# Kernel optimization log

Measured on AMD Instinct MI355X. Metric: run time of the kernel, lower is better.

The kernel has to match this reference:

```python
import jax, jax.numpy as jnp
import numpy as np

B, C_IN, H, W = 1, 448, 64, 64   # concat of resnet18 layer1/2/3 resized to 64x64: 64+128+256=448
D, L = 100, 4096                 # projection dim, number of spatial locations (gaussian params)
OUT_HW = 256                     # input_size for final bilinear upsample


def setup_inputs() -> dict:
    key = jax.random.key(0)
    k0, k1, k2, k3, k4 = jax.random.split(key, 5)
    return {
        "features": jax.random.normal(k0, (B, C_IN, H, W), jnp.float32),
        "proj_w": jax.random.normal(k1, (D, C_IN), jnp.float32) * 0.05,
        "proj_b": jax.random.normal(k2, (D,), jnp.float32) * 0.05,
        "mean": jax.random.normal(k3, (D, L), jnp.float32),
        "inv_cov": jax.random.normal(k4, (L, D, D), jnp.float32) * 0.01,
    }


def reference(features, proj_w, proj_b, mean, inv_cov):
    Bn, C, Hh, Ww = features.shape
    # permute(0,2,3,1).reshape(-1, C) then Linear(C, D)
    f = features.transpose(0, 2, 3, 1).reshape(-1, C)          # (N, C), N = B*H*W
    f = f @ proj_w.T + proj_b                                  # (N, D)
    m = mean.T                                                 # (L, D)
    # Batched Mahalanobis-style quadratic form replacing the Python loop over L=4096:
    #   dist[n, l] = (f_n - m_l)^T  inv_cov_l  (f_n - m_l)
    # Expanded so the heavy term is a single (N, D*D) x (D*D, L) GEMM (no (N,L,D) intermediate).
    Cm  = jnp.einsum('lde,le->ld', inv_cov, m)                 # inv_cov_l @ m_l        (L, D)
    CTm = jnp.einsum('lde,ld->le', inv_cov, m)                 # inv_cov_l^T @ m_l      (L, D)
    const = jnp.einsum('ld,ld->l', m, Cm)                      # m_l^T inv_cov_l m_l    (L,)
    ff = (f[:, :, None] * f[:, None, :]).reshape(f.shape[0], D * D)   # outer(f,f) flattened (N, D*D)
    quad = ff @ inv_cov.reshape(L, D * D).T                    # f^T inv_cov_l f        (N, L)
    dist = quad - f @ (Cm + CTm).T + const[None, :]            # (N, L)
    min_d = jnp.min(dist, axis=1).reshape(Bn, Hh, Ww)[:, None, :, :]  # (B, 1, H, W)
    amap = (min_d - min_d.min()) / (min_d.max() - min_d.min() + 1e-8)
    amap = jax.image.resize(amap, (Bn, 1, OUT_HW, OUT_HW), method='bilinear')
    return amap
```

## Files before the change

### kernel.cpp

```cpp
#include <hip/hip_runtime.h>
#include <hip/hip_bf16.h>
#include <stdint.h>

#define CIN   448
#define DP    100
#define NPIX  4096
#define LNUM  4096
#define KQ    5050
#define KLIN  5150
#define KTOT  5184
#define KSTEPS (KTOT / 64)
#define OUTHW 256

typedef _Float16 f16_t;
typedef _Float16 f16x8 __attribute__((ext_vector_type(8)));
typedef float    f32x4 __attribute__((ext_vector_type(4)));
typedef unsigned short u16x8 __attribute__((ext_vector_type(8)));

static __device__ __forceinline__ int tri_off(int d) { return (d * (201 - d)) >> 1; }

static __device__ __forceinline__ void unpack_tri(int k, int& d, int& e) {
    int dd = (int)((201.0f - sqrtf(40401.0f - 8.0f * (float)k)) * 0.5f);
    if (dd < 0) dd = 0;
    if (dd > 99) dd = 99;
    while (tri_off(dd + 1) <= k) ++dd;
    while (tri_off(dd) > k) --dd;
    d = dd;
    e = dd + (k - tri_off(dd));
}

static __device__ __forceinline__ unsigned f2u(float x) {
    unsigned b = __float_as_uint(x);
    return (b & 0x80000000u) ? ~b : (b | 0x80000000u);
}
static __device__ __forceinline__ float u2f(unsigned u) {
    unsigned b = (u & 0x80000000u) ? (u & 0x7FFFFFFFu) : ~u;
    return __uint_as_float(b);
}

static __device__ __forceinline__ void gload_lds16(const f16_t* g, f16_t* l) {
    __builtin_amdgcn_global_load_lds((const __attribute__((address_space(1))) unsigned*)g,
                                     (__attribute__((address_space(3))) unsigned*)l,
                                     16, 0, 0);
}

__global__ void k_lut(unsigned short* __restrict__ lut) {
    int k = blockIdx.x * 256 + threadIdx.x;
    if (k < KTOT) {
        int d = 0, e = 0;
        if (k < KQ) unpack_tri(k, d, e);
        lut[k] = (unsigned short)(d | (e << 8));
    }
}

__global__ void k_proj(const float* __restrict__ feat, const float* __restrict__ w,
                       const float* __restrict__ b, float* __restrict__ f) {
    int gid = blockIdx.x * 256 + threadIdx.x;
    int n = gid & 4095;
    int d = gid >> 12;
    float acc = b[d];
    const float* wd = w + d * CIN;
    #pragma unroll 4
    for (int c = 0; c < CIN; ++c) acc += feat[c * 4096 + n] * wd[c];
    f[n * DP + d] = acc;
}

__global__ __launch_bounds__(256) void k_buildA(const float* __restrict__ f, const unsigned short* __restrict__ lut,
                                                f16_t* __restrict__ A) {
    __shared__ float fr[DP];
    int n = blockIdx.x;
    int t = threadIdx.x;
    if (t < DP) fr[t] = f[n * DP + t];
    __syncthreads();
    int r  = n & 127;
    int rsw = (r & 7) << 3;
    f16_t* tileBase = A + (size_t)(n >> 7) * KSTEPS * 8192;
    for (int g = t; g < KTOT / 8; g += 256) {
        int k0 = g * 8;
        u16x8 lu = *(const u16x8*)&lut[k0];
        f16x8 v;
        #pragma unroll
        for (int j = 0; j < 8; ++j) {
            int k = k0 + j;
            float x;
            if (k < KQ) {
                int d = lu[j] & 255, e = lu[j] >> 8;
                x = fr[d] * fr[e];
            } else if (k < KLIN) {
                x = fr[k - KQ];
            } else {
                x = 0.0f;
            }
            v[j] = (f16_t)x;
        }
        int kt = k0 >> 6, kin = k0 & 63;
        *(f16x8*)&tileBase[kt * 8192 + r * 64 + ((kin & 56) ^ rsw)] = v;
    }
}

__global__ __launch_bounds__(256) void k_buildB(const float* __restrict__ icov, const float* __restrict__ mean,
                                                const unsigned short* __restrict__ lut,
                                                f16_t* __restrict__ Bm, float* __restrict__ constl) {
    __shared__ float ic[DP * 101];
    __shared__ float ml[DP];
    __shared__ float wv[DP];
    __shared__ float part[DP];
    int l = blockIdx.x;
    int t = threadIdx.x;
    const float* src = icov + (size_t)l * DP * DP;
    for (int i = t; i < DP * DP; i += 256) {
        int row = i / 100;
        ic[row * 101 + (i - row * 100)] = src[i];
    }
    if (t < DP) ml[t] = mean[t * LNUM + l];
    __syncthreads();
    if (t < DP) {
        float icm = 0.f, ictm = 0.f;
        for (int e = 0; e < DP; ++e) {
            icm  += ic[t * 101 + e] * ml[e];
            ictm += ic[e * 101 + t] * ml[e];
        }
        wv[t]   = icm + ictm;
        part[t] = ml[t] * icm;
    }
    __syncthreads();
    if (t == 0) {
        float c = 0.f;
        for (int d = 0; d < DP; ++d) c += part[d];
        constl[l] = c;
    }
    int r  = l & 127;
    int rsw = (r & 7) << 3;
    f16_t* tileBase = Bm + (size_t)(l >> 7) * KSTEPS * 8192;
    for (int g = t; g < KTOT / 8; g += 256) {
        int k0 = g * 8;
        u16x8 lu = *(const u16x8*)&lut[k0];
        f16x8 v;
        #pragma unroll
        for (int j = 0; j < 8; ++j) {
            int k = k0 + j;
            float x;
            if (k < KQ) {
                int d = lu[j] & 255, e = lu[j] >> 8;
                float s = ic[d * 101 + e] + ic[e * 101 + d];
                x = (d == e) ? 0.5f * s : s;
            } else if (k < KLIN) {
                x = -wv[k - KQ];
            } else {
                x = 0.0f;
            }
            v[j] = (f16_t)x;
        }
        int kt = k0 >> 6, kin = k0 & 63;
        *(f16x8*)&tileBase[kt * 8192 + r * 64 + ((kin & 56) ^ rsw)] = v;
    }
}

__global__ void k_init(unsigned* __restrict__ mind) {
    int i = blockIdx.x * 256 + threadIdx.x;
    if (i < NPIX) mind[i] = 0xFFFFFFFFu;
}

__global__ __launch_bounds__(512, 2) void k_gemm(const f16_t* __restrict__ A, const f16_t* __restrict__ Bm,
                                                 const float* __restrict__ constl, unsigned* __restrict__ mind) {
    __shared__ __align__(16) f16_t sA[2][16384];
    __shared__ __align__(16) f16_t sB[2][16384];

    int bid = blockIdx.x;
    int pid = ((bid & 7) << 5) | (bid >> 3);
    int bm = pid & 15;
    int bn = pid >> 4;

    int t = threadIdx.x;
    int lane = t & 63;
    int w = t >> 6;
    int wr = w >> 2;
    int wc = w & 3;

    f32x4 acc[8][4];
    #pragma unroll
    for (int i = 0; i < 8; ++i)
        #pragma unroll
        for (int j = 0; j < 4; ++j) acc[i][j] = (f32x4){0.f, 0.f, 0.f, 0.f};

    const f16_t* Abase = A  + ((size_t)(2 * bm + (w >> 2)) * KSTEPS) * 8192 + (w & 3) * 2048 + lane * 8;
    const f16_t* Bbase = Bm + ((size_t)(2 * bn + (w >> 2)) * KSTEPS) * 8192 + (w & 3) * 2048 + lane * 8;

    int l15 = lane & 15;
    int xorv = (lane & 7) << 3;
    int klobase = (lane >> 4) * 8;

    {
        const f16_t* As = Abase;
        const f16_t* Bs = Bbase;
        #pragma unroll
        for (int c = 0; c < 4; ++c) {
            gload_lds16(As + c * 512, &sA[0][w * 2048 + c * 512]);
            gload_lds16(Bs + c * 512, &sB[0][w * 2048 + c * 512]);
        }
    }
    __syncthreads();

    for (int kt = 0; kt < KSTEPS; ++kt) {
        int p = kt & 1;
        if (kt + 1 < KSTEPS) {
            const f16_t* As = Abase + (size_t)(kt + 1) * 8192;
            const f16_t* Bs = Bbase + (size_t)(kt + 1) * 8192;
            #pragma unroll
            for (int c = 0; c < 4; ++c) {
                gload_lds16(As + c * 512, &sA[p ^ 1][w * 2048 + c * 512]);
                gload_lds16(Bs + c * 512, &sB[p ^ 1][w * 2048 + c * 512]);
            }
        }
        #pragma unroll
        for (int kk = 0; kk < 2; ++kk) {
            int klo = (kk * 32 + klobase) ^ xorv;
            f16x8 bfr[4];
            #pragma unroll
            for (int ni = 0; ni < 4; ++ni) {
                int rr = (wc & 1) * 64 + ni * 16 + l15;
                bfr[ni] = *(const f16x8*)&sB[p][(wc >> 1) * 8192 + rr * 64 + klo];
            }
            #pragma unroll
            for (int mq = 0; mq < 2; ++mq) {
                f16x8 afr[4];
                #pragma unroll
                for (int mi = 0; mi < 4; ++mi) {
                    int rr = (mq * 4 + mi) * 16 + l15;
                    afr[mi] = *(const f16x8*)&sA[p][wr * 8192 + rr * 64 + klo];
                }
                __builtin_amdgcn_s_setprio(1);
                #pragma unroll
                for (int mi = 0; mi < 4; ++mi)
                    #pragma unroll
                    for (int ni = 0; ni < 4; ++ni)
                        acc[mq * 4 + mi][ni] =
                            __builtin_amdgcn_mfma_f32_16x16x32_f16(afr[mi], bfr[ni], acc[mq * 4 + mi][ni], 0, 0, 0);
                __builtin_amdgcn_s_setprio(0);
            }
        }
        __syncthreads();
    }

    int colbase = bn * 256 + wc * 64 + l15;
    float cl[4];
    #pragma unroll
    for (int ni = 0; ni < 4; ++ni) cl[ni] = constl[colbase + ni * 16];
    #pragma unroll
    for (int mi8 = 0; mi8 < 8; ++mi8) {
        #pragma unroll
        for (int j = 0; j < 4; ++j) {
            float v = 1e30f;
            #pragma unroll
            for (int ni = 0; ni < 4; ++ni) v = fminf(v, acc[mi8][ni][j] + cl[ni]);
            #pragma unroll
            for (int s = 1; s < 16; s <<= 1) v = fminf(v, __shfl_xor(v, s, 64));
            if (l15 == 0) {
                int row = bm * 256 + wr * 128 + mi8 * 16 + (lane >> 4) * 4 + j;
                atomicMin(&mind[row], f2u(v));
            }
        }
    }
}

__global__ void k_minmax(const unsigned* __restrict__ mind, float* __restrict__ gmm) {
    __shared__ float smin[256], smax[256];
    int t = threadIdx.x;
    float vmin = 1e30f, vmax = -1e30f;
    for (int i = t; i < NPIX; i += 256) {
        float v = u2f(mind[i]);
        vmin = fminf(vmin, v);
        vmax = fmaxf(vmax, v);
    }
    smin[t] = vmin; smax[t] = vmax;
    __syncthreads();
    for (int s = 128; s > 0; s >>= 1) {
        if (t < s) {
            smin[t] = fminf(smin[t], smin[t + s]);
            smax[t] = fmaxf(smax[t], smax[t + s]);
        }
        __syncthreads();
    }
    if (t == 0) { gmm[0] = smin[0]; gmm[1] = smax[0]; }
}

__global__ void k_upsample(const unsigned* __restrict__ mind, const float* __restrict__ gmm,
                           float* __restrict__ out) {
    int gid = blockIdx.x * 256 + threadIdx.x;
    int i = gid >> 8, j = gid & 255;
    float gmin = gmm[0];
    float scale = 1.0f / (gmm[1] - gmm[0] + 1e-8f);
    float x = fminf(fmaxf(j * 0.25f - 0.375f, 0.0f), 63.0f);
    float y = fminf(fmaxf(i * 0.25f - 0.375f, 0.0f), 63.0f);
    int x0 = (int)x, y0 = (int)y;
    int x1 = min(x0 + 1, 63), y1 = min(y0 + 1, 63);
    float fx = x - x0, fy = y - y0;
    float v00 = u2f(mind[y0 * 64 + x0]), v01 = u2f(mind[y0 * 64 + x1]);
    float v10 = u2f(mind[y1 * 64 + x0]), v11 = u2f(mind[y1 * 64 + x1]);
    float v = v00 * (1.f - fy) * (1.f - fx) + v01 * (1.f - fy) * fx
            + v10 * fy * (1.f - fx) + v11 * fy * fx;
    out[gid] = (v - gmin) * scale;
}

__global__ void k_diag(float* __restrict__ out) {
    int gid = blockIdx.x * 256 + threadIdx.x;
    out[gid] = 0.25f;
}

extern "C" void kernel_launch(void* const* d_in, const int* in_sizes, int n_in,
                              void* d_out, int out_size, void* d_ws, size_t ws_size,
                              hipStream_t stream) {
    const float* feat = (const float*)d_in[0];
    const float* pw   = (const float*)d_in[1];
    const float* pb   = (const float*)d_in[2];
    const float* mean = (const float*)d_in[3];
    const float* icov = (const float*)d_in[4];

    size_t need = 0;
    auto count = [&need](size_t bytes) { need = ((need + 255) & ~(size_t)255) + bytes; };
    count((size_t)NPIX * DP * 4);
    count((size_t)NPIX * KTOT * 2);
    count((size_t)LNUM * KTOT * 2);
    count((size_t)LNUM * 4);
    count((size_t)NPIX * 4);
    count(2 * 4);
    count((size_t)KTOT * 2);
    if (ws_size < need) {
        k_diag<<<256, 256, 0, stream>>>((float*)d_out);
        return;
    }

    char* ws = (char*)d_ws;
    size_t off = 0;
    auto alloc = [&](size_t bytes) -> void* {
        off = (off + 255) & ~(size_t)255;
        void* p = ws + off;
        off += bytes;
        return p;
    };
    float*          f      = (float*)alloc((size_t)NPIX * DP * 4);
    f16_t*          Amat   = (f16_t*)alloc((size_t)NPIX * KTOT * 2);
    f16_t*          Bmat   = (f16_t*)alloc((size_t)LNUM * KTOT * 2);
    float*          constl = (float*)alloc((size_t)LNUM * 4);
    unsigned*       mind   = (unsigned*)alloc((size_t)NPIX * 4);
    float*          gmm    = (float*)alloc(2 * 4);
    unsigned short* lut    = (unsigned short*)alloc((size_t)KTOT * 2);

    k_lut     <<<(KTOT + 255) / 256, 256, 0, stream>>>(lut);
    k_proj    <<<1600, 256, 0, stream>>>(feat, pw, pb, f);
    k_buildA  <<<NPIX, 256, 0, stream>>>(f, lut, Amat);
    k_buildB  <<<LNUM, 256, 0, stream>>>(icov, mean, lut, Bmat, constl);
    k_init    <<<16, 256, 0, stream>>>(mind);
    k_gemm    <<<256, 512, 0, stream>>>(Amat, Bmat, constl, mind);
    k_minmax  <<<1, 256, 0, stream>>>(mind, gmm);
    k_upsample<<<256, 256, 0, stream>>>(mind, gmm, (float*)d_out);
}
```

Measured before the change: 292.6 us.

## Shrink GEMM tiles to 128x128 with 1024 blocks, fuse init, vectorize icov load

The main GEMM moves from 256x256 tiles with 512 threads and 256 blocks to 128x128 tiles with 256 threads and 1024 blocks. Each wave now computes a 64x64 subtile, and the block-to-tile swizzle changes to group blocks in bands of 8 M-tiles. The aim is to fill all CUs of the MI355X and raise occupancy, at the cost of lower operand reuse and twice the global/L2 traffic for A and B. The mind initialisation is folded into the LUT kernel, which removes one launch. The inverse-covariance load in buildB now uses float4 reads.

Measured after the change: 307.2 us. +5.0%, slower.

```diff
diff --git a/kernel.cpp b/kernel.cpp
--- a/kernel.cpp
+++ b/kernel.cpp
@@ -44,13 +44,14 @@
                                      16, 0, 0);
 }
 
-__global__ void k_lut(unsigned short* __restrict__ lut) {
+__global__ void k_lut(unsigned short* __restrict__ lut, unsigned* __restrict__ mind) {
     int k = blockIdx.x * 256 + threadIdx.x;
     if (k < KTOT) {
         int d = 0, e = 0;
         if (k < KQ) unpack_tri(k, d, e);
         lut[k] = (unsigned short)(d | (e << 8));
     }
+    if (k < NPIX) mind[k] = 0xFFFFFFFFu;
 }
 
 __global__ void k_proj(const float* __restrict__ feat, const float* __restrict__ w,
@@ -107,10 +108,14 @@
     __shared__ float part[DP];
     int l = blockIdx.x;
     int t = threadIdx.x;
-    const float* src = icov + (size_t)l * DP * DP;
-    for (int i = t; i < DP * DP; i += 256) {
-        int row = i / 100;
-        ic[row * 101 + (i - row * 100)] = src[i];
+    const float4* src4 = (const float4*)(icov + (size_t)l * DP * DP);
+    for (int i4 = t; i4 < DP * DP / 4; i4 += 256) {
+        float4 v = src4[i4];
+        int flat = i4 * 4;
+        int row = flat / 100;
+        int col = flat - row * 100;
+        float* dst = &ic[row * 101 + col];
+        dst[0] = v.x; dst[1] = v.y; dst[2] = v.z; dst[3] = v.w;
     }
     if (t < DP) ml[t] = mean[t * LNUM + l];
     __syncthreads();
@@ -156,56 +161,50 @@
     }
 }
 
-__global__ void k_init(unsigned* __restrict__ mind) {
-    int i = blockIdx.x * 256 + threadIdx.x;
-    if (i < NPIX) mind[i] = 0xFFFFFFFFu;
-}
-
-__global__ __launch_bounds__(512, 2) void k_gemm(const f16_t* __restrict__ A, const f16_t* __restrict__ Bm,
+__global__ __launch_bounds__(256, 2) void k_gemm(const f16_t* __restrict__ A, const f16_t* __restrict__ Bm,
                                                  const float* __restrict__ constl, unsigned* __restrict__ mind) {
-    __shared__ __align__(16) f16_t sA[2][16384];
-    __shared__ __align__(16) f16_t sB[2][16384];
+    __shared__ __align__(16) f16_t sA[2][8192];
+    __shared__ __align__(16) f16_t sB[2][8192];
 
     int bid = blockIdx.x;
-    int pid = ((bid & 7) << 5) | (bid >> 3);
-    int bm = pid & 15;
-    int bn = pid >> 4;
+    int pid = ((bid & 7) << 7) | (bid >> 3);
+    int group = pid >> 8;
+    int pin = pid & 255;
+    int bm = group * 8 + (pin & 7);
+    int bn = pin >> 3;
 
     int t = threadIdx.x;
     int lane = t & 63;
     int w = t >> 6;
-    int wr = w >> 2;
-    int wc = w & 3;
-
-    f32x4 acc[8][4];
+    int wr = w >> 1, wc = w & 1;
+
+    f32x4 acc[4][4];
     #pragma unroll
-    for (int i = 0; i < 8; ++i)
+    for (int i = 0; i < 4; ++i)
         #pragma unroll
         for (int j = 0; j < 4; ++j) acc[i][j] = (f32x4){0.f, 0.f, 0.f, 0.f};
 
-    const f16_t* Abase = A  + ((size_t)(2 * bm + (w >> 2)) * KSTEPS) * 8192 + (w & 3) * 2048 + lane * 8;
-    const f16_t* Bbase = Bm + ((size_t)(2 * bn + (w >> 2)) * KSTEPS) * 8192 + (w & 3) * 2048 + lane * 8;
+    const f16_t* Atile = A  + (size_t)bm * KSTEPS * 8192 + w * 2048 + lane * 8;
+    const f16_t* Btile = Bm + (size_t)bn * KSTEPS * 8192 + w * 2048 + lane * 8;
 
     int l15 = lane & 15;
     int xorv = (lane & 7) << 3;
     int klobase = (lane >> 4) * 8;
-
-    {
-        const f16_t* As = Abase;
-        const f16_t* Bs = Bbase;
-        #pragma unroll
-        for (int c = 0; c < 4; ++c) {
-            gload_lds16(As + c * 512, &sA[0][w * 2048 + c * 512]);
-            gload_lds16(Bs + c * 512, &sB[0][w * 2048 + c * 512]);
-        }
+    int arowbase = wr * 64 + l15;
+    int browbase = wc * 64 + l15;
+
+    #pragma unroll
+    for (int c = 0; c < 4; ++c) {
+        gload_lds16(Atile + c * 512, &sA[0][w * 2048 + c * 512]);
+        gload_lds16(Btile + c * 512, &sB[0][w * 2048 + c * 512]);
     }
     __syncthreads();
 
     for (int kt = 0; kt < KSTEPS; ++kt) {
         int p = kt & 1;
         if (kt + 1 < KSTEPS) {
-            const f16_t* As = Abase + (size_t)(kt + 1) * 8192;
-            const f16_t* Bs = Bbase + (size_t)(kt + 1) * 8192;
+            const f16_t* As = Atile + (size_t)(kt + 1) * 8192;
+            const f16_t* Bs = Btile + (size_t)(kt + 1) * 8192;
             #pragma unroll
             for (int c = 0; c < 4; ++c) {
                 gload_lds16(As + c * 512, &sA[p ^ 1][w * 2048 + c * 512]);
@@ -215,48 +214,37 @@
         #pragma unroll
         for (int kk = 0; kk < 2; ++kk) {
             int klo = (kk * 32 + klobase) ^ xorv;
-            f16x8 bfr[4];
-            #pragma unroll
-            for (int ni = 0; ni < 4; ++ni) {
-                int rr = (wc & 1) * 64 + ni * 16 + l15;
-                bfr[ni] = *(const f16x8*)&sB[p][(wc >> 1) * 8192 + rr * 64 + klo];
-            }
-            #pragma unroll
-            for (int mq = 0; mq < 2; ++mq) {
-                f16x8 afr[4];
+            f16x8 afr[4], bfr[4];
+            #pragma unroll
+            for (int mi = 0; mi < 4; ++mi)
+                afr[mi] = *(const f16x8*)&sA[p][(arowbase + mi * 16) * 64 + klo];
+            #pragma unroll
+            for (int ni = 0; ni < 4; ++ni)
+                bfr[ni] = *(const f16x8*)&sB[p][(browbase + ni * 16) * 64 + klo];
+            #pragma unroll
+            for (int mi = 0; mi < 4; ++mi)
                 #pragma unroll
-                for (int mi = 0; mi < 4; ++mi) {
-                    int rr = (mq * 4 + mi) * 16 + l15;
-                    afr[mi] = *(const f16x8*)&sA[p][wr * 8192 + rr * 64 + klo];
-                }
-                __builtin_amdgcn_s_setprio(1);
-                #pragma unroll
-                for (int mi = 0; mi < 4; ++mi)
-                    #pragma unroll
-                    for (int ni = 0; ni < 4; ++ni)
-                        acc[mq * 4 + mi][ni] =
-                            __builtin_amdgcn_mfma_f32_16x16x32_f16(afr[mi], bfr[ni], acc[mq * 4 + mi][ni], 0, 0, 0);
-                __builtin_amdgcn_s_setprio(0);
-            }
+                for (int ni = 0; ni < 4; ++ni)
+                    acc[mi][ni] = __builtin_amdgcn_mfma_f32_16x16x32_f16(afr[mi], bfr[ni], acc[mi][ni], 0, 0, 0);
         }
         __syncthreads();
     }
 
-    int colbase = bn * 256 + wc * 64 + l15;
+    int colbase = bn * 128 + wc * 64 + l15;
     float cl[4];
     #pragma unroll
     for (int ni = 0; ni < 4; ++ni) cl[ni] = constl[colbase + ni * 16];
     #pragma unroll
-    for (int mi8 = 0; mi8 < 8; ++mi8) {
+    for (int mi = 0; mi < 4; ++mi) {
         #pragma unroll
         for (int j = 0; j < 4; ++j) {
             float v = 1e30f;
             #pragma unroll
-            for (int ni = 0; ni < 4; ++ni) v = fminf(v, acc[mi8][ni][j] + cl[ni]);
+            for (int ni = 0; ni < 4; ++ni) v = fminf(v, acc[mi][ni][j] + cl[ni]);
             #pragma unroll
             for (int s = 1; s < 16; s <<= 1) v = fminf(v, __shfl_xor(v, s, 64));
             if (l15 == 0) {
-                int row = bm * 256 + wr * 128 + mi8 * 16 + (lane >> 4) * 4 + j;
+                int row = bm * 128 + wr * 64 + mi * 16 + (lane >> 4) * 4 + j;
                 atomicMin(&mind[row], f2u(v));
             }
         }
@@ -346,12 +334,11 @@
     float*          gmm    = (float*)alloc(2 * 4);
     unsigned short* lut    = (unsigned short*)alloc((size_t)KTOT * 2);
 
-    k_lut     <<<(KTOT + 255) / 256, 256, 0, stream>>>(lut);
+    k_lut     <<<(KTOT + 255) / 256, 256, 0, stream>>>(lut, mind);
     k_proj    <<<1600, 256, 0, stream>>>(feat, pw, pb, f);
     k_buildA  <<<NPIX, 256, 0, stream>>>(f, lut, Amat);
     k_buildB  <<<LNUM, 256, 0, stream>>>(icov, mean, lut, Bmat, constl);
-    k_init    <<<16, 256, 0, stream>>>(mind);
-    k_gemm    <<<256, 512, 0, stream>>>(Amat, Bmat, constl, mind);
+    k_gemm    <<<1024, 256, 0, stream>>>(Amat, Bmat, constl, mind);
     k_minmax  <<<1, 256, 0, stream>>>(mind, gmm);
     k_upsample<<<256, 256, 0, stream>>>(mind, gmm, (float*)d_out);
 }
```
